# Optimization experiments

Hardware: AMD Instinct MI355X
Metric: run time of the kernel (lower is better)

Reference implementation:

```python
import jax, jax.numpy as jnp
import numpy as np

B, T, EMB, H = 8, 1024, 128, 8


def setup_inputs() -> dict:
    key = jax.random.key(0)
    ks = jax.random.split(key, 7)
    s = 0.02
    return {
        "x": jax.random.normal(ks[0], (B, T, EMB), dtype=jnp.float32),
        "mask": jax.random.randint(ks[1], (1, T, T), 0, 2, dtype=jnp.int32),
        "Wk": (jax.random.normal(ks[2], (EMB * H, EMB), dtype=jnp.float32) * s),
        "Wq": (jax.random.normal(ks[3], (EMB * H, EMB), dtype=jnp.float32) * s),
        "Wv": (jax.random.normal(ks[4], (EMB * H, EMB), dtype=jnp.float32) * s),
        "Wu": (jax.random.normal(ks[5], (EMB, EMB * H), dtype=jnp.float32) * s),
        "bu": (jax.random.normal(ks[6], (EMB,), dtype=jnp.float32) * s),
    }


def reference(x, mask, Wk, Wq, Wv, Wu, bu):
    b, t, e = x.shape  # e == emb; per-head dim also == emb in this module
    h = Wk.shape[0] // e
    # projections: (b,t,e) @ (e, h*e) -> (b,t,h,e) -> (b,h,t,e)
    q = (x @ Wq.T).reshape(b, t, h, e).transpose(0, 2, 1, 3)
    k = (x @ Wk.T).reshape(b, t, h, e).transpose(0, 2, 1, 3)
    v = (x @ Wv.T).reshape(b, t, h, e).transpose(0, 2, 1, 3)
    scale = e ** 0.25  # torch scales q and k each by e**(1/4)
    dot = jnp.einsum('bhqe,bhke->bhqk', q / scale, k / scale)
    # causal mask: strictly-upper triangle (offset=1) set to -inf FIRST
    causal = jnp.triu(jnp.ones((t, t), dtype=bool), k=1)
    dot = jnp.where(causal, -jnp.inf, dot)
    # padding mask: where mask==0 set to -1e9 (overwrites -inf where overlapping)
    dot = jnp.where(mask[:, None] == 0, jnp.float32(-1e9), dot)
    attn = jax.nn.softmax(dot, axis=-1)
    out = jnp.einsum('bhqk,bhke->bhqe', attn, v)
    out = out.transpose(0, 2, 1, 3).reshape(b, t, h * e)
    return out @ Wu.T + bu
```

## Files before the change

kernel.cpp:

```cpp
#include <hip/hip_runtime.h>

#define Bn 8
#define Hn 8
#define Tn 1024
#define Dn 128

typedef __attribute__((ext_vector_type(8))) short bf16x8;
typedef __attribute__((ext_vector_type(4))) float f32x4;

typedef __attribute__((address_space(3))) unsigned int lds_as_t;
typedef __attribute__((address_space(1))) const unsigned int glb_as_t;

static __device__ __forceinline__ void gload_lds16(const unsigned short* g, unsigned short* l) {
    __builtin_amdgcn_global_load_lds((glb_as_t*)g, (lds_as_t*)l, 16, 0, 0);
}

static __device__ __forceinline__ unsigned short f2bf(float f) {
    union { float f; unsigned int u; } v; v.f = f;
    unsigned int u = v.u;
    return (unsigned short)((u + 0x7FFFu + ((u >> 16) & 1u)) >> 16);
}

__global__ __launch_bounds__(256) void prep_kernel(
    const float* __restrict__ x,  const float* __restrict__ Wq,
    const float* __restrict__ Wk, const float* __restrict__ Wv,
    const float* __restrict__ Wu, const int* __restrict__ mask,
    unsigned short* __restrict__ xb,  unsigned short* __restrict__ wqB,
    unsigned short* __restrict__ wkB, unsigned short* __restrict__ wvB,
    unsigned short* __restrict__ wuB, unsigned long long* __restrict__ bits)
{
    const int blk = blockIdx.x;
    const int tid = threadIdx.x;

    if (blk < 1408) {
        const float* in; unsigned short* out; int i4;
        if (blk < 1024)      { in = x;  out = xb;  i4 = blk * 256 + tid; }
        else if (blk < 1152) { in = Wq; out = wqB; i4 = (blk - 1024) * 256 + tid; }
        else if (blk < 1280) { in = Wk; out = wkB; i4 = (blk - 1152) * 256 + tid; }
        else                 { in = Wv; out = wvB; i4 = (blk - 1280) * 256 + tid; }
        float4 f = ((const float4*)in)[i4];
        ushort4 o;
        o.x = f2bf(f.x); o.y = f2bf(f.y); o.z = f2bf(f.z); o.w = f2bf(f.w);
        int base = i4 * 4;
        int row = base >> 7, col = base & 127;
        int scol = (((col >> 3) ^ (row & 15)) << 3) | (col & 7);
        *(ushort4*)(out + row * 128 + scol) = o;
    } else if (blk < 1536) {
        int i4 = (blk - 1408) * 256 + tid;
        float4 f = ((const float4*)Wu)[i4];
        ushort4 o;
        o.x = f2bf(f.x); o.y = f2bf(f.y); o.z = f2bf(f.z); o.w = f2bf(f.w);
        ((ushort4*)wuB)[i4] = o;
    } else {
        int wid  = (blk - 1536) * 4 + (tid >> 6);
        int lane = tid & 63;
#pragma unroll
        for (int i = 0; i < 4; i++) {
            int widx = wid * 4 + i;
            int row = widx >> 4, kt = widx & 15;
            int v = mask[row * Tn + kt * 64 + lane];
            unsigned long long b = __ballot(v != 0);
            if (lane == 0) bits[widx] = b;
        }
    }
}

__global__ __launch_bounds__(256, 2) void qkv_kernel(
    const unsigned short* __restrict__ xb,
    const unsigned short* __restrict__ wqB,
    const unsigned short* __restrict__ wkB,
    const unsigned short* __restrict__ wvB,
    unsigned short* __restrict__ Q,
    unsigned short* __restrict__ K,
    unsigned short* __restrict__ Vt)
{
    const int bx = blockIdx.x, by = blockIdx.y;
    const int wave = threadIdx.x >> 6;
    const int lane = threadIdx.x & 63;
    const int l16  = lane & 15;
    const int quad = lane >> 4;
    const int wm = wave & 1, wn = wave >> 1;

    __shared__ __align__(16) unsigned short As[128 * 128];
    __shared__ __align__(16) unsigned short Bs[128 * 128];

    const int which = by >> 3;
    const unsigned short* wsel = (which == 0) ? wqB : (which == 1) ? wkB : wvB;
    const unsigned short* Ag = xb + (size_t)bx * 128 * 128;
    const unsigned short* Bg = wsel + (size_t)(by & 7) * 128 * 128;

#pragma unroll
    for (int i = 0; i < 8; i++) {
        int base = (wave * 8 + i) * 512;
        gload_lds16(Ag + base + lane * 8, &As[base]);
        gload_lds16(Bg + base + lane * 8, &Bs[base]);
    }
    __syncthreads();

    bf16x8 a[4][4];
#pragma unroll
    for (int mt = 0; mt < 4; mt++) {
        int row = wm * 64 + mt * 16 + l16;
#pragma unroll
        for (int ks = 0; ks < 4; ks++)
            a[mt][ks] = *(const bf16x8*)(&As[row * 128 + (((ks * 4 + quad) ^ (row & 15)) << 3)]);
    }

    f32x4 acc[4][4];
#pragma unroll
    for (int nt = 0; nt < 4; nt++) {
        int row = wn * 64 + nt * 16 + l16;
        bf16x8 b4[4];
#pragma unroll
        for (int ks = 0; ks < 4; ks++)
            b4[ks] = *(const bf16x8*)(&Bs[row * 128 + (((ks * 4 + quad) ^ (row & 15)) << 3)]);
#pragma unroll
        for (int mt = 0; mt < 4; mt++) {
            f32x4 c = {0.f, 0.f, 0.f, 0.f};
#pragma unroll
            for (int ks = 0; ks < 4; ks++)
                c = __builtin_amdgcn_mfma_f32_16x16x32_bf16(a[mt][ks], b4[ks], c, 0, 0, 0);
            acc[mt][nt] = c;
        }
    }

    const int h_ = by & 7;
#pragma unroll
    for (int mt = 0; mt < 4; mt++) {
        int m_base = bx * 128 + wm * 64 + mt * 16 + quad * 4;
        int b_ = m_base >> 10;
        int t0 = m_base & 1023;
#pragma unroll
        for (int nt = 0; nt < 4; nt++) {
            int ncol = wn * 64 + nt * 16 + l16;
            if (which == 2) {
                int kt_ = t0 >> 6, tc0 = t0 & 63;
                int e_ = ncol;
                size_t off = ((((size_t)(b_ * Hn + h_) * 16 + kt_) * 128 + e_) << 6)
                           + ((((tc0 >> 3) ^ (e_ & 7)) << 3) | (tc0 & 7));
                ushort4 v4;
                v4.x = f2bf(acc[mt][nt][0]); v4.y = f2bf(acc[mt][nt][1]);
                v4.z = f2bf(acc[mt][nt][2]); v4.w = f2bf(acc[mt][nt][3]);
                *(ushort4*)(Vt + off) = v4;
            } else {
#pragma unroll
                for (int r = 0; r < 4; r++) {
                    int t_ = t0 + r;
                    unsigned short v = f2bf(acc[mt][nt][r]);
                    size_t rowoff = ((size_t)((b_ * Hn + h_) * Tn + t_)) * Dn;
                    if (which == 0) {
                        Q[rowoff + ncol] = v;
                    } else {
                        int nc = ((((ncol >> 3) ^ (t_ & 15)) << 3) | (ncol & 7));
                        K[rowoff + nc] = v;
                    }
                }
            }
        }
    }
}

__global__ __launch_bounds__(256, 2) void attn_kernel(
    const unsigned short* __restrict__ Q,
    const unsigned short* __restrict__ K,
    const unsigned short* __restrict__ Vt,
    const unsigned long long* __restrict__ mbits,
    unsigned short* __restrict__ AO)
{
    const int qt   = 15 - ((blockIdx.x + blockIdx.y) & 15);
    const int bh   = blockIdx.y;
    const int wave = threadIdx.x >> 6;
    const int lane = threadIdx.x & 63;
    const int l16  = lane & 15;
    const int quad = lane >> 4;

    __shared__ __align__(16) unsigned short kbuf[2][64 * 128];
    __shared__ __align__(16) unsigned short vbuf[2][128 * 64];
    __shared__ __align__(16) unsigned short pbuf[4][16][72];

    const unsigned short* Qb = Q  + (size_t)bh * Tn * Dn;
    const unsigned short* Kb = K  + (size_t)bh * Tn * Dn;
    const unsigned short* Vb = Vt + (size_t)bh * (16 * 128 * 64);

    const int q0 = qt * 64 + wave * 16;
    const int qrow = q0 + quad * 4;
    const unsigned long long* mrow = mbits + (size_t)qrow * 16;

    bf16x8 qf[4];
#pragma unroll
    for (int ks = 0; ks < 4; ks++)
        qf[ks] = *(const bf16x8*)(Qb + (size_t)(q0 + l16) * Dn + ks * 32 + quad * 8);

    bf16x8 ones;
#pragma unroll
    for (int j = 0; j < 8; j++) ones[j] = (short)0x3F80;

    f32x4 o[8];
#pragma unroll
    for (int et = 0; et < 8; et++) o[et] = (f32x4){0.f, 0.f, 0.f, 0.f};
    f32x4 lacc = {0.f, 0.f, 0.f, 0.f};

    const float SL = 0.12752041570284543f;

#pragma unroll
    for (int i = 0; i < 4; i++) {
        int base = (wave * 4 + i) * 512;
        gload_lds16(Kb + base + lane * 8, &kbuf[0][base]);
        gload_lds16(Vb + base + lane * 8, &vbuf[0][base]);
    }

    for (int kt = 0; kt <= qt; kt++) {
        const int cur = kt & 1;
        __syncthreads();

        if (kt < qt) {
            const unsigned short* Kg = Kb + (kt + 1) * (64 * 128);
            const unsigned short* Vg = Vb + (kt + 1) * (128 * 64);
#pragma unroll
            for (int i = 0; i < 4; i++) {
                int base = (wave * 4 + i) * 512;
                gload_lds16(Kg + base + lane * 8, &kbuf[cur ^ 1][base]);
                gload_lds16(Vg + base + lane * 8, &vbuf[cur ^ 1][base]);
            }
        }

        unsigned long long mw[4];
#pragma unroll
        for (int r = 0; r < 4; r++) mw[r] = mrow[r * 16 + kt];

        f32x4 s[4];
#pragma unroll
        for (int nt = 0; nt < 4; nt++) {
            bf16x8 b4[4];
#pragma unroll
            for (int ks = 0; ks < 4; ks++)
                b4[ks] = *(const bf16x8*)(&kbuf[cur][(nt * 16 + l16) * 128 + (((ks * 4 + quad) ^ l16) << 3)]);
            f32x4 c = {0.f, 0.f, 0.f, 0.f};
#pragma unroll
            for (int ks = 0; ks < 4; ks++)
                c = __builtin_amdgcn_mfma_f32_16x16x32_bf16(qf[ks], b4[ks], c, 0, 0, 0);
            s[nt] = c;
        }

        const int kc0 = kt * 64;
#pragma unroll
        for (int nt = 0; nt < 4; nt++) {
            int bi = nt * 16 + l16;
            int key = kc0 + bi;
#pragma unroll
            for (int r = 0; r < 4; r++) {
                bool live = ((mw[r] >> bi) & 1ULL) && !(kt == qt && key > qrow + r);
                float p = live ? __builtin_amdgcn_exp2f(s[nt][r] * SL) : 0.f;
                pbuf[wave][quad * 4 + r][bi] = f2bf(p);
            }
        }

        bf16x8 pf[2];
#pragma unroll
        for (int k2 = 0; k2 < 2; k2++)
            pf[k2] = *(const bf16x8*)(&pbuf[wave][l16][k2 * 32 + quad * 8]);

#pragma unroll
        for (int k2 = 0; k2 < 2; k2++)
            lacc = __builtin_amdgcn_mfma_f32_16x16x32_bf16(pf[k2], ones, lacc, 0, 0, 0);
#pragma unroll
        for (int et = 0; et < 8; et++) {
            f32x4 c = o[et];
#pragma unroll
            for (int k2 = 0; k2 < 2; k2++) {
                bf16x8 b = *(const bf16x8*)(&vbuf[cur][(et * 16 + l16) * 64 + (((k2 * 4 + quad) ^ (l16 & 7)) << 3)]);
                c = __builtin_amdgcn_mfma_f32_16x16x32_bf16(pf[k2], b, c, 0, 0, 0);
            }
            o[et] = c;
        }
    }

    {
        bool deg = (lacc[0] == 0.f) | (lacc[1] == 0.f) | (lacc[2] == 0.f) | (lacc[3] == 0.f);
        if (__ballot(deg) != 0ULL) {
            unsigned short dsel[4];
#pragma unroll
            for (int r = 0; r < 4; r++) dsel[r] = (lacc[r] == 0.f) ? (unsigned short)0x3F80 : (unsigned short)0;
            for (int kt = 0; kt < 16; kt++) {
                unsigned long long mw[4];
#pragma unroll
                for (int r = 0; r < 4; r++) mw[r] = mrow[r * 16 + kt];
#pragma unroll
                for (int nt = 0; nt < 4; nt++) {
                    int bi = nt * 16 + l16;
#pragma unroll
                    for (int r = 0; r < 4; r++)
                        pbuf[wave][quad * 4 + r][bi] = ((mw[r] >> bi) & 1ULL) ? (unsigned short)0 : dsel[r];
                }
                bf16x8 pf[2];
#pragma unroll
                for (int k2 = 0; k2 < 2; k2++)
                    pf[k2] = *(const bf16x8*)(&pbuf[wave][l16][k2 * 32 + quad * 8]);
#pragma unroll
                for (int k2 = 0; k2 < 2; k2++)
                    lacc = __builtin_amdgcn_mfma_f32_16x16x32_bf16(pf[k2], ones, lacc, 0, 0, 0);
#pragma unroll
                for (int et = 0; et < 8; et++) {
                    f32x4 c = o[et];
#pragma unroll
                    for (int k2 = 0; k2 < 2; k2++) {
                        const unsigned short* vg = Vb + kt * (128 * 64)
                            + (et * 16 + l16) * 64 + (((k2 * 4 + quad) ^ (l16 & 7)) << 3);
                        bf16x8 b = *(const bf16x8*)vg;
                        c = __builtin_amdgcn_mfma_f32_16x16x32_bf16(pf[k2], b, c, 0, 0, 0);
                    }
                    o[et] = c;
                }
            }
        }
    }

    const int b_ = bh >> 3, h_ = bh & 7;
#pragma unroll
    for (int r = 0; r < 4; r++) {
        float inv = 1.f / lacc[r];
        int q = qrow + r;
        size_t rowoff = (size_t)(b_ * Tn + q) * (Hn * Dn) + h_ * Dn;
#pragma unroll
        for (int et = 0; et < 8; et++)
            AO[rowoff + et * 16 + l16] = f2bf(o[et][r] * inv);
    }
}

__global__ void zero_kernel(float4* __restrict__ p, int n4) {
    int i = blockIdx.x * blockDim.x + threadIdx.x;
    if (i < n4) p[i] = (float4){0.f, 0.f, 0.f, 0.f};
}

__global__ __launch_bounds__(256) void outproj_kernel(
    const unsigned short* __restrict__ AO,
    const unsigned short* __restrict__ wuB,
    const float* __restrict__ bu,
    float* __restrict__ out)
{
    const int wave = threadIdx.x >> 6;
    const int lane = threadIdx.x & 63;
    const int l16  = lane & 15;
    const int quad = lane >> 4;
    const int m0 = blockIdx.x * 64 + wave * 16;
    const int ks0 = blockIdx.y * 16;

    f32x4 acc[8];
#pragma unroll
    for (int nt = 0; nt < 8; nt++) acc[nt] = (f32x4){0.f, 0.f, 0.f, 0.f};

    for (int g = 0; g < 4; g++) {
        int kk = ks0 + g * 4;
        bf16x8 a4[4];
#pragma unroll
        for (int j = 0; j < 4; j++)
            a4[j] = *(const bf16x8*)(AO + (size_t)(m0 + l16) * 1024 + (kk + j) * 32 + quad * 8);
#pragma unroll
        for (int nt = 0; nt < 8; nt++) {
            bf16x8 b4[4];
#pragma unroll
            for (int j = 0; j < 4; j++)
                b4[j] = *(const bf16x8*)(wuB + (size_t)(nt * 16 + l16) * 1024 + (kk + j) * 32 + quad * 8);
#pragma unroll
            for (int j = 0; j < 4; j++)
                acc[nt] = __builtin_amdgcn_mfma_f32_16x16x32_bf16(a4[j], b4[j], acc[nt], 0, 0, 0);
        }
    }

#pragma unroll
    for (int nt = 0; nt < 8; nt++) {
        int n = nt * 16 + l16;
        float bias = (blockIdx.y == 0) ? bu[n] : 0.f;
#pragma unroll
        for (int r = 0; r < 4; r++) {
            int m = m0 + quad * 4 + r;
            atomicAdd(&out[(size_t)m * Dn + n], acc[nt][r] + bias);
        }
    }
}

extern "C" void kernel_launch(void* const* d_in, const int* in_sizes, int n_in,
                              void* d_out, int out_size, void* d_ws, size_t ws_size,
                              hipStream_t stream) {
    const float* x   = (const float*)d_in[0];
    const int* mask  = (const int*)d_in[1];
    const float* Wk  = (const float*)d_in[2];
    const float* Wq  = (const float*)d_in[3];
    const float* Wv  = (const float*)d_in[4];
    const float* Wu  = (const float*)d_in[5];
    const float* bu  = (const float*)d_in[6];
    float* out = (float*)d_out;

    char* ws = (char*)d_ws;
    unsigned short* xb  = (unsigned short*)ws; ws += (size_t)8192 * 128 * 2;
    unsigned short* wqB = (unsigned short*)ws; ws += (size_t)1024 * 128 * 2;
    unsigned short* wkB = (unsigned short*)ws; ws += (size_t)1024 * 128 * 2;
    unsigned short* wvB = (unsigned short*)ws; ws += (size_t)1024 * 128 * 2;
    unsigned short* wuB = (unsigned short*)ws; ws += (size_t)128 * 1024 * 2;
    unsigned short* Qw  = (unsigned short*)ws; ws += (size_t)64 * 1024 * 128 * 2;
    unsigned short* Kw  = (unsigned short*)ws; ws += (size_t)64 * 1024 * 128 * 2;
    unsigned short* Vtw = (unsigned short*)ws; ws += (size_t)64 * 1024 * 128 * 2;
    unsigned short* AOw = (unsigned short*)ws; ws += (size_t)8192 * 1024 * 2;
    unsigned long long* mb = (unsigned long long*)ws; ws += (size_t)1024 * 16 * 8;

    prep_kernel<<<dim3(2560), 256, 0, stream>>>(x, Wq, Wk, Wv, Wu, mask,
                                                xb, wqB, wkB, wvB, wuB, mb);
    zero_kernel<<<dim3(1024), 256, 0, stream>>>((float4*)out, 8192 * 128 / 4);
    qkv_kernel<<<dim3(64, 24), 256, 0, stream>>>(xb, wqB, wkB, wvB, Qw, Kw, Vtw);
    attn_kernel<<<dim3(16, 64), 256, 0, stream>>>(Qw, Kw, Vtw, mb, AOw);
    outproj_kernel<<<dim3(128, 2), 256, 0, stream>>>(AOw, wuB, bu, out);
}
```

Baseline: 179.6 us.

## Process two query subtiles per wave in attention; reduce outproj splits in LDS

The attention kernel now gives each block 128 query rows (32 per wave, two 16-row subtiles). Each K/V tile loaded into LDS is reused across twice as many queries, and blocks are ordered on a 1D grid that pairs heavy and light causal tiles. The output projection drops the split-K atomics and the zero-fill kernel: each block handles 16 rows, splits K across its four waves, and sums the partials in LDS before a plain store with bias. In exchange, registers per thread roughly double (two sets of O accumulators), which may lower occupancy, and the number of attention blocks halves.

```diff
diff --git a/kernel.cpp b/kernel.cpp
--- a/kernel.cpp
+++ b/kernel.cpp
@@ -167,8 +167,9 @@
     const unsigned long long* __restrict__ mbits,
     unsigned short* __restrict__ AO)
 {
-    const int qt   = 15 - ((blockIdx.x + blockIdx.y) & 15);
-    const int bh   = blockIdx.y;
+    const int id   = blockIdx.x;
+    const int qb   = (id & 7) ^ (7 * ((id >> 8) & 1));
+    const int bh   = (id >> 3) & 63;
     const int wave = threadIdx.x >> 6;
     const int lane = threadIdx.x & 63;
     const int l16  = lane & 15;
@@ -182,23 +183,28 @@
     const unsigned short* Kb = K  + (size_t)bh * Tn * Dn;
     const unsigned short* Vb = Vt + (size_t)bh * (16 * 128 * 64);
 
-    const int q0 = qt * 64 + wave * 16;
-    const int qrow = q0 + quad * 4;
-    const unsigned long long* mrow = mbits + (size_t)qrow * 16;
-
-    bf16x8 qf[4];
-#pragma unroll
-    for (int ks = 0; ks < 4; ks++)
-        qf[ks] = *(const bf16x8*)(Qb + (size_t)(q0 + l16) * Dn + ks * 32 + quad * 8);
+    const int ktmax = 2 * qb + 1;
+    const int q0 = qb * 128 + wave * 32;
+
+    bf16x8 qf[2][4];
+#pragma unroll
+    for (int st = 0; st < 2; st++)
+#pragma unroll
+        for (int ks = 0; ks < 4; ks++)
+            qf[st][ks] = *(const bf16x8*)(Qb + (size_t)(q0 + st * 16 + l16) * Dn + ks * 32 + quad * 8);
 
     bf16x8 ones;
 #pragma unroll
     for (int j = 0; j < 8; j++) ones[j] = (short)0x3F80;
 
-    f32x4 o[8];
-#pragma unroll
-    for (int et = 0; et < 8; et++) o[et] = (f32x4){0.f, 0.f, 0.f, 0.f};
-    f32x4 lacc = {0.f, 0.f, 0.f, 0.f};
+    f32x4 o[2][8];
+#pragma unroll
+    for (int st = 0; st < 2; st++)
+#pragma unroll
+        for (int et = 0; et < 8; et++) o[st][et] = (f32x4){0.f, 0.f, 0.f, 0.f};
+    f32x4 lacc[2];
+    lacc[0] = (f32x4){0.f, 0.f, 0.f, 0.f};
+    lacc[1] = (f32x4){0.f, 0.f, 0.f, 0.f};
 
     const float SL = 0.12752041570284543f;
 
@@ -209,11 +215,11 @@
         gload_lds16(Vb + base + lane * 8, &vbuf[0][base]);
     }
 
-    for (int kt = 0; kt <= qt; kt++) {
+    for (int kt = 0; kt <= ktmax; kt++) {
         const int cur = kt & 1;
         __syncthreads();
 
-        if (kt < qt) {
+        if (kt < ktmax) {
             const unsigned short* Kg = Kb + (kt + 1) * (64 * 128);
             const unsigned short* Vg = Vb + (kt + 1) * (128 * 64);
 #pragma unroll
@@ -224,92 +230,117 @@
             }
         }
 
-        unsigned long long mw[4];
-#pragma unroll
-        for (int r = 0; r < 4; r++) mw[r] = mrow[r * 16 + kt];
-
-        f32x4 s[4];
+        unsigned long long mw[2][4];
+#pragma unroll
+        for (int st = 0; st < 2; st++)
+#pragma unroll
+            for (int r = 0; r < 4; r++)
+                mw[st][r] = mbits[(size_t)(q0 + st * 16 + quad * 4 + r) * 16 + kt];
+
+        f32x4 s[2][4];
 #pragma unroll
         for (int nt = 0; nt < 4; nt++) {
             bf16x8 b4[4];
 #pragma unroll
             for (int ks = 0; ks < 4; ks++)
                 b4[ks] = *(const bf16x8*)(&kbuf[cur][(nt * 16 + l16) * 128 + (((ks * 4 + quad) ^ l16) << 3)]);
-            f32x4 c = {0.f, 0.f, 0.f, 0.f};
-#pragma unroll
-            for (int ks = 0; ks < 4; ks++)
-                c = __builtin_amdgcn_mfma_f32_16x16x32_bf16(qf[ks], b4[ks], c, 0, 0, 0);
-            s[nt] = c;
+#pragma unroll
+            for (int st = 0; st < 2; st++) {
+                f32x4 c = {0.f, 0.f, 0.f, 0.f};
+#pragma unroll
+                for (int ks = 0; ks < 4; ks++)
+                    c = __builtin_amdgcn_mfma_f32_16x16x32_bf16(qf[st][ks], b4[ks], c, 0, 0, 0);
+                s[st][nt] = c;
+            }
         }
 
         const int kc0 = kt * 64;
-#pragma unroll
-        for (int nt = 0; nt < 4; nt++) {
-            int bi = nt * 16 + l16;
-            int key = kc0 + bi;
-#pragma unroll
-            for (int r = 0; r < 4; r++) {
-                bool live = ((mw[r] >> bi) & 1ULL) && !(kt == qt && key > qrow + r);
-                float p = live ? __builtin_amdgcn_exp2f(s[nt][r] * SL) : 0.f;
-                pbuf[wave][quad * 4 + r][bi] = f2bf(p);
-            }
-        }
-
-        bf16x8 pf[2];
-#pragma unroll
-        for (int k2 = 0; k2 < 2; k2++)
-            pf[k2] = *(const bf16x8*)(&pbuf[wave][l16][k2 * 32 + quad * 8]);
-
-#pragma unroll
-        for (int k2 = 0; k2 < 2; k2++)
-            lacc = __builtin_amdgcn_mfma_f32_16x16x32_bf16(pf[k2], ones, lacc, 0, 0, 0);
+        bf16x8 pf[2][2];
+#pragma unroll
+        for (int st = 0; st < 2; st++) {
+#pragma unroll
+            for (int nt = 0; nt < 4; nt++) {
+                int bi = nt * 16 + l16;
+                int key = kc0 + bi;
+#pragma unroll
+                for (int r = 0; r < 4; r++) {
+                    int q = q0 + st * 16 + quad * 4 + r;
+                    bool live = ((mw[st][r] >> bi) & 1ULL) && (key <= q);
+                    float p = live ? __builtin_amdgcn_exp2f(s[st][nt][r] * SL) : 0.f;
+                    pbuf[wave][quad * 4 + r][bi] = f2bf(p);
+                }
+            }
+#pragma unroll
+            for (int k2 = 0; k2 < 2; k2++)
+                pf[st][k2] = *(const bf16x8*)(&pbuf[wave][l16][k2 * 32 + quad * 8]);
+        }
+
+#pragma unroll
+        for (int st = 0; st < 2; st++)
+#pragma unroll
+            for (int k2 = 0; k2 < 2; k2++)
+                lacc[st] = __builtin_amdgcn_mfma_f32_16x16x32_bf16(pf[st][k2], ones, lacc[st], 0, 0, 0);
+
 #pragma unroll
         for (int et = 0; et < 8; et++) {
-            f32x4 c = o[et];
 #pragma unroll
             for (int k2 = 0; k2 < 2; k2++) {
                 bf16x8 b = *(const bf16x8*)(&vbuf[cur][(et * 16 + l16) * 64 + (((k2 * 4 + quad) ^ (l16 & 7)) << 3)]);
-                c = __builtin_amdgcn_mfma_f32_16x16x32_bf16(pf[k2], b, c, 0, 0, 0);
-            }
-            o[et] = c;
+                o[0][et] = __builtin_amdgcn_mfma_f32_16x16x32_bf16(pf[0][k2], b, o[0][et], 0, 0, 0);
+                o[1][et] = __builtin_amdgcn_mfma_f32_16x16x32_bf16(pf[1][k2], b, o[1][et], 0, 0, 0);
+            }
         }
     }
 
     {
-        bool deg = (lacc[0] == 0.f) | (lacc[1] == 0.f) | (lacc[2] == 0.f) | (lacc[3] == 0.f);
+        bool deg = false;
+#pragma unroll
+        for (int st = 0; st < 2; st++)
+#pragma unroll
+            for (int r = 0; r < 4; r++) deg |= (lacc[st][r] == 0.f);
         if (__ballot(deg) != 0ULL) {
-            unsigned short dsel[4];
-#pragma unroll
-            for (int r = 0; r < 4; r++) dsel[r] = (lacc[r] == 0.f) ? (unsigned short)0x3F80 : (unsigned short)0;
+            unsigned short dsel[2][4];
+#pragma unroll
+            for (int st = 0; st < 2; st++)
+#pragma unroll
+                for (int r = 0; r < 4; r++)
+                    dsel[st][r] = (lacc[st][r] == 0.f) ? (unsigned short)0x3F80 : (unsigned short)0;
             for (int kt = 0; kt < 16; kt++) {
-                unsigned long long mw[4];
-#pragma unroll
-                for (int r = 0; r < 4; r++) mw[r] = mrow[r * 16 + kt];
-#pragma unroll
-                for (int nt = 0; nt < 4; nt++) {
-                    int bi = nt * 16 + l16;
+                unsigned long long mw[2][4];
+#pragma unroll
+                for (int st = 0; st < 2; st++)
 #pragma unroll
                     for (int r = 0; r < 4; r++)
-                        pbuf[wave][quad * 4 + r][bi] = ((mw[r] >> bi) & 1ULL) ? (unsigned short)0 : dsel[r];
+                        mw[st][r] = mbits[(size_t)(q0 + st * 16 + quad * 4 + r) * 16 + kt];
+                bf16x8 pf[2][2];
+#pragma unroll
+                for (int st = 0; st < 2; st++) {
+#pragma unroll
+                    for (int nt = 0; nt < 4; nt++) {
+                        int bi = nt * 16 + l16;
+#pragma unroll
+                        for (int r = 0; r < 4; r++)
+                            pbuf[wave][quad * 4 + r][bi] = ((mw[st][r] >> bi) & 1ULL) ? (unsigned short)0 : dsel[st][r];
+                    }
+#pragma unroll
+                    for (int k2 = 0; k2 < 2; k2++)
+                        pf[st][k2] = *(const bf16x8*)(&pbuf[wave][l16][k2 * 32 + quad * 8]);
                 }
-                bf16x8 pf[2];
-#pragma unroll
-                for (int k2 = 0; k2 < 2; k2++)
-                    pf[k2] = *(const bf16x8*)(&pbuf[wave][l16][k2 * 32 + quad * 8]);
-#pragma unroll
-                for (int k2 = 0; k2 < 2; k2++)
-                    lacc = __builtin_amdgcn_mfma_f32_16x16x32_bf16(pf[k2], ones, lacc, 0, 0, 0);
+#pragma unroll
+                for (int st = 0; st < 2; st++)
+#pragma unroll
+                    for (int k2 = 0; k2 < 2; k2++)
+                        lacc[st] = __builtin_amdgcn_mfma_f32_16x16x32_bf16(pf[st][k2], ones, lacc[st], 0, 0, 0);
 #pragma unroll
                 for (int et = 0; et < 8; et++) {
-                    f32x4 c = o[et];
 #pragma unroll
                     for (int k2 = 0; k2 < 2; k2++) {
                         const unsigned short* vg = Vb + kt * (128 * 64)
                             + (et * 16 + l16) * 64 + (((k2 * 4 + quad) ^ (l16 & 7)) << 3);
                         bf16x8 b = *(const bf16x8*)vg;
-                        c = __builtin_amdgcn_mfma_f32_16x16x32_bf16(pf[k2], b, c, 0, 0, 0);
+                        o[0][et] = __builtin_amdgcn_mfma_f32_16x16x32_bf16(pf[0][k2], b, o[0][et], 0, 0, 0);
+                        o[1][et] = __builtin_amdgcn_mfma_f32_16x16x32_bf16(pf[1][k2], b, o[1][et], 0, 0, 0);
                     }
-                    o[et] = c;
                 }
             }
         }
@@ -317,19 +348,16 @@
 
     const int b_ = bh >> 3, h_ = bh & 7;
 #pragma unroll
-    for (int r = 0; r < 4; r++) {
-        float inv = 1.f / lacc[r];
-        int q = qrow + r;
-        size_t rowoff = (size_t)(b_ * Tn + q) * (Hn * Dn) + h_ * Dn;
-#pragma unroll
-        for (int et = 0; et < 8; et++)
-            AO[rowoff + et * 16 + l16] = f2bf(o[et][r] * inv);
-    }
-}
-
-__global__ void zero_kernel(float4* __restrict__ p, int n4) {
-    int i = blockIdx.x * blockDim.x + threadIdx.x;
-    if (i < n4) p[i] = (float4){0.f, 0.f, 0.f, 0.f};
+    for (int st = 0; st < 2; st++)
+#pragma unroll
+        for (int r = 0; r < 4; r++) {
+            float inv = 1.f / lacc[st][r];
+            int q = q0 + st * 16 + quad * 4 + r;
+            size_t rowoff = (size_t)(b_ * Tn + q) * (Hn * Dn) + h_ * Dn;
+#pragma unroll
+            for (int et = 0; et < 8; et++)
+                AO[rowoff + et * 16 + l16] = f2bf(o[st][et][r] * inv);
+        }
 }
 
 __global__ __launch_bounds__(256) void outproj_kernel(
@@ -342,40 +370,46 @@
     const int lane = threadIdx.x & 63;
     const int l16  = lane & 15;
     const int quad = lane >> 4;
-    const int m0 = blockIdx.x * 64 + wave * 16;
-    const int ks0 = blockIdx.y * 16;
+    const int m0 = blockIdx.x * 16;
+
+    __shared__ float red[4][16][128];
 
     f32x4 acc[8];
 #pragma unroll
     for (int nt = 0; nt < 8; nt++) acc[nt] = (f32x4){0.f, 0.f, 0.f, 0.f};
 
-    for (int g = 0; g < 4; g++) {
-        int kk = ks0 + g * 4;
-        bf16x8 a4[4];
-#pragma unroll
-        for (int j = 0; j < 4; j++)
-            a4[j] = *(const bf16x8*)(AO + (size_t)(m0 + l16) * 1024 + (kk + j) * 32 + quad * 8);
+    const int kk0 = wave * 8;
+#pragma unroll
+    for (int g = 0; g < 8; g++) {
+        int kk = kk0 + g;
+        bf16x8 a = *(const bf16x8*)(AO + (size_t)(m0 + l16) * 1024 + kk * 32 + quad * 8);
 #pragma unroll
         for (int nt = 0; nt < 8; nt++) {
-            bf16x8 b4[4];
-#pragma unroll
-            for (int j = 0; j < 4; j++)
-                b4[j] = *(const bf16x8*)(wuB + (size_t)(nt * 16 + l16) * 1024 + (kk + j) * 32 + quad * 8);
-#pragma unroll
-            for (int j = 0; j < 4; j++)
-                acc[nt] = __builtin_amdgcn_mfma_f32_16x16x32_bf16(a4[j], b4[j], acc[nt], 0, 0, 0);
-        }
-    }
-
-#pragma unroll
-    for (int nt = 0; nt < 8; nt++) {
-        int n = nt * 16 + l16;
-        float bias = (blockIdx.y == 0) ? bu[n] : 0.f;
-#pragma unroll
-        for (int r = 0; r < 4; r++) {
-            int m = m0 + quad * 4 + r;
-            atomicAdd(&out[(size_t)m * Dn + n], acc[nt][r] + bias);
-        }
+            bf16x8 b = *(const bf16x8*)(wuB + (size_t)(nt * 16 + l16) * 1024 + kk * 32 + quad * 8);
+            acc[nt] = __builtin_amdgcn_mfma_f32_16x16x32_bf16(a, b, acc[nt], 0, 0, 0);
+        }
+    }
+
+#pragma unroll
+    for (int nt = 0; nt < 8; nt++)
+#pragma unroll
+        for (int r = 0; r < 4; r++)
+            red[wave][quad * 4 + r][nt * 16 + l16] = acc[nt][r];
+    __syncthreads();
+
+#pragma unroll
+    for (int i = 0; i < 2; i++) {
+        int flat = threadIdx.x * 2 + i;
+        int row = flat >> 5, c4 = (flat & 31) * 4;
+        f32x4 v = *(const f32x4*)(&red[0][row][c4]);
+#pragma unroll
+        for (int w = 1; w < 4; w++) {
+            f32x4 p = *(const f32x4*)(&red[w][row][c4]);
+            v[0] += p[0]; v[1] += p[1]; v[2] += p[2]; v[3] += p[3];
+        }
+        float4 bb = *(const float4*)(bu + c4);
+        v[0] += bb.x; v[1] += bb.y; v[2] += bb.z; v[3] += bb.w;
+        *(f32x4*)(out + (size_t)(m0 + row) * Dn + c4) = v;
     }
 }
 
@@ -405,8 +439,7 @@
 
     prep_kernel<<<dim3(2560), 256, 0, stream>>>(x, Wq, Wk, Wv, Wu, mask,
                                                 xb, wqB, wkB, wvB, wuB, mb);
-    zero_kernel<<<dim3(1024), 256, 0, stream>>>((float4*)out, 8192 * 128 / 4);
     qkv_kernel<<<dim3(64, 24), 256, 0, stream>>>(xb, wqB, wkB, wvB, Qw, Kw, Vtw);
-    attn_kernel<<<dim3(16, 64), 256, 0, stream>>>(Qw, Kw, Vtw, mb, AOw);
-    outproj_kernel<<<dim3(128, 2), 256, 0, stream>>>(AOw, wuB, bu, out);
-}
+    attn_kernel<<<dim3(512), 256, 0, stream>>>(Qw, Kw, Vtw, mb, AOw);
+    outproj_kernel<<<dim3(512), 256, 0, stream>>>(AOw, wuB, bu, out);
+}
```

Result: faster. 163.0 us (-9.2%).
